# Optimization experiments

Hardware: AMD Instinct MI355X
Metric: run time of the kernel (lower is better)

Reference implementation:

```python
import jax, jax.numpy as jnp
import numpy as np

NUM_EMBEDDINGS = 1024
EMBEDDING_DIM = 64
COMMITMENT_COST = 0.25


def setup_inputs() -> dict:
    key = jax.random.key(0)
    k_x, k_cb = jax.random.split(key)
    x = jax.random.normal(k_x, (16, EMBEDDING_DIM, 64, 64), dtype=jnp.float32)
    # nn.Embedding weight init: uniform(-1/K, 1/K)
    codebook = jax.random.uniform(
        k_cb, (NUM_EMBEDDINGS, EMBEDDING_DIM), dtype=jnp.float32,
        minval=-1.0 / NUM_EMBEDDINGS, maxval=1.0 / NUM_EMBEDDINGS)
    return {"x": x, "codebook": codebook}


def reference(x, codebook):
    sg = jax.lax.stop_gradient
    # NCHW -> NHWC
    inputs = jnp.transpose(x, (0, 2, 3, 1))  # [B,H,W,D]
    in_shape = inputs.shape
    flat = inputs.reshape(-1, EMBEDDING_DIM)  # [N,D]
    # squared L2 distances to each codebook entry: [N,K]
    distances = (jnp.sum(flat ** 2, axis=1, keepdims=True)
                 + jnp.sum(codebook ** 2, axis=1)
                 - 2.0 * jnp.matmul(flat, codebook.T))
    encoding_indices = jnp.argmin(distances, axis=1)  # [N]
    # one-hot matmul in the original == plain gather
    quantized = codebook[encoding_indices].reshape(in_shape)  # [B,H,W,D]
    e_latent_loss = jnp.mean((sg(quantized) - inputs) ** 2)
    q_latent_loss = jnp.mean((quantized - sg(inputs)) ** 2)
    loss = q_latent_loss + COMMITMENT_COST * e_latent_loss
    # straight-through estimator
    quantized = inputs + sg(quantized - inputs)
    quantized = jnp.transpose(quantized, (0, 3, 1, 2))  # NHWC -> NCHW
    return quantized, loss
```

## Files before the change

### kernel.cpp

```cpp
#include <hip/hip_runtime.h>

#define NPTS   65536
#define DIM    64
#define KCODES 1024
#define HW     4096
#define ROWP   68

typedef __attribute__((ext_vector_type(8))) short  short8;
typedef __attribute__((ext_vector_type(4))) float  floatx4;
typedef __attribute__((ext_vector_type(2))) unsigned long long ull2;

__device__ __forceinline__ short f2bf(float f) {
    unsigned u = __builtin_bit_cast(unsigned, f);
    u = (u + 0x7FFFu + ((u >> 16) & 1u)) >> 16;
    return (short)u;
}
__device__ __forceinline__ float bf2f(short s) {
    unsigned u = ((unsigned)(unsigned short)s) << 16;
    return __builtin_bit_cast(float, u);
}

__global__ void vq_prep(const float* __restrict__ cb, float* __restrict__ cbn_nh,
                        float* __restrict__ loss_ptr) {
    int k = blockIdx.x * blockDim.x + threadIdx.x;
    if (k == 0) *loss_ptr = 0.0f;
    if (k < KCODES) {
        const float* row = cb + (size_t)k * DIM;
        float s = 0.0f;
        #pragma unroll
        for (int d = 0; d < DIM; ++d) s = fmaf(row[d], row[d], s);
        cbn_nh[k] = -0.5f * s;
    }
}

__global__ __launch_bounds__(256, 1) void vq_main(
    const float* __restrict__ x, const float* __restrict__ cb,
    const float* __restrict__ cbn_nh, float* __restrict__ out,
    float* __restrict__ loss_ptr)
{
    __shared__ __align__(16) short s_cb[KCODES * ROWP];
    __shared__ float s_cbn[KCODES];
    __shared__ int   s_idx[256];
    __shared__ float s_red[4];

    const int tid  = threadIdx.x;
    const int lane = tid & 63;
    const int wave = tid >> 6;
    const int col  = lane & 15;
    const int quad = lane >> 4;

    {
        const float4* src = (const float4*)cb;
        for (int i = 0; i < 64; ++i) {
            int f4 = tid + 256 * i;
            float4 v = src[f4];
            int e = f4 << 2;
            int code = e >> 6, within = e & 63;
            unsigned long long p =
                ((unsigned long long)(unsigned short)f2bf(v.x)) |
                ((unsigned long long)(unsigned short)f2bf(v.y) << 16) |
                ((unsigned long long)(unsigned short)f2bf(v.z) << 32) |
                ((unsigned long long)(unsigned short)f2bf(v.w) << 48);
            *(unsigned long long*)&s_cb[code * ROWP + within] = p;
        }
        #pragma unroll
        for (int i = 0; i < 4; ++i) s_cbn[tid + 256 * i] = cbn_nh[tid + 256 * i];
    }

    const int p0 = blockIdx.x * 256 + wave * 64;
    short8 afrag[4][2];
    #pragma unroll
    for (int blk = 0; blk < 4; ++blk) {
        int n = p0 + blk * 16 + col;
        const float* bp = x + ((size_t)(n >> 12) << 18) + (n & 4095);
        #pragma unroll
        for (int kh = 0; kh < 2; ++kh) {
            int dbase = kh * 32 + quad * 8;
            short8 f;
            #pragma unroll
            for (int j = 0; j < 8; ++j)
                f[j] = f2bf(bp[(size_t)(dbase + j) * HW]);
            afrag[blk][kh] = f;
        }
    }
    __syncthreads();

    float best[4][4];
    #pragma unroll
    for (int blk = 0; blk < 4; ++blk)
        #pragma unroll
        for (int r = 0; r < 4; ++r) best[blk][r] = -3.4e38f;

    for (int t = 0; t < 64; ++t) {
        const int cbase = t * 16;
        const int code  = cbase + col;
        const float initv = s_cbn[code];
        const unsigned idxv = (unsigned)code;
        const short* rp = &s_cb[code * ROWP + quad * 8];
        ull2 u0; u0.x = *(const unsigned long long*)rp;
        u0.y = *(const unsigned long long*)(rp + 4);
        ull2 u1; u1.x = *(const unsigned long long*)(rp + 32);
        u1.y = *(const unsigned long long*)(rp + 36);
        const short8 b0 = __builtin_bit_cast(short8, u0);
        const short8 b1 = __builtin_bit_cast(short8, u1);
        floatx4 cinit = {initv, initv, initv, initv};
        #pragma unroll
        for (int blk = 0; blk < 4; ++blk) {
            floatx4 acc = __builtin_amdgcn_mfma_f32_16x16x32_bf16(afrag[blk][0], b0, cinit, 0, 0, 0);
            acc = __builtin_amdgcn_mfma_f32_16x16x32_bf16(afrag[blk][1], b1, acc, 0, 0, 0);
            #pragma unroll
            for (int r = 0; r < 4; ++r) {
                unsigned pb = (__builtin_bit_cast(unsigned, acc[r]) & 0xFFFFFC00u) | idxv;
                best[blk][r] = fmaxf(best[blk][r], __builtin_bit_cast(float, pb));
            }
        }
    }

    #pragma unroll
    for (int blk = 0; blk < 4; ++blk)
        #pragma unroll
        for (int r = 0; r < 4; ++r) {
            float v = best[blk][r];
            v = fmaxf(v, __shfl_xor(v, 1, 64));
            v = fmaxf(v, __shfl_xor(v, 2, 64));
            v = fmaxf(v, __shfl_xor(v, 4, 64));
            v = fmaxf(v, __shfl_xor(v, 8, 64));
            best[blk][r] = v;
        }
    if (col == 0) {
        #pragma unroll
        for (int blk = 0; blk < 4; ++blk)
            #pragma unroll
            for (int r = 0; r < 4; ++r)
                s_idx[wave * 64 + blk * 16 + quad * 4 + r] =
                    (int)(__builtin_bit_cast(unsigned, best[blk][r]) & 1023u);
    }

    {
        int n = p0 + lane;
        int idx = s_idx[wave * 64 + lane];
        size_t base = ((size_t)(n >> 12) << 18) + (n & 4095);
        float* op = out + base;
        const float* xp = x + base;
        float lsum = 0.0f;
        #pragma unroll
        for (int j = 0; j < 16; ++j) {
            unsigned long long u = *(const unsigned long long*)&s_cb[idx * ROWP + j * 4];
            #pragma unroll
            for (int e = 0; e < 4; ++e) {
                float c = bf2f((short)(u >> (16 * e)));
                int d = j * 4 + e;
                float xv = xp[(size_t)d * HW];
                op[(size_t)d * HW] = c;
                float diff = xv - c;
                lsum = fmaf(diff, diff, lsum);
            }
        }
        #pragma unroll
        for (int off = 32; off > 0; off >>= 1)
            lsum += __shfl_down(lsum, off, 64);
        if (lane == 0) s_red[wave] = lsum;
    }
    __syncthreads();
    if (tid == 0) {
        float s = (s_red[0] + s_red[1]) + (s_red[2] + s_red[3]);
        atomicAdd(loss_ptr, s * (1.25f / (float)((size_t)NPTS * DIM)));
    }
}

extern "C" void kernel_launch(void* const* d_in, const int* in_sizes, int n_in,
                              void* d_out, int out_size, void* d_ws, size_t ws_size,
                              hipStream_t stream) {
    const float* x  = (const float*)d_in[0];
    const float* cb = (const float*)d_in[1];
    float* out      = (float*)d_out;
    float* cbn      = (float*)d_ws;
    float* loss_ptr = out + (size_t)NPTS * DIM;

    vq_prep<<<KCODES / 256, 256, 0, stream>>>(cb, cbn, loss_ptr);
    vq_main<<<NPTS / 256, 256, 0, stream>>>(x, cb, cbn, out, loss_ptr);
}
```

Measured before the change: 97.59 us.

## Use 1024-thread blocks with one 16-point tile per wave, fold norms in

Each block now runs 16 waves instead of 4. Every wave handles a single 16-point MFMA tile instead of four, which spreads the 256 points and the codebook staging over four times as many threads. The separate codebook-norm prep kernel is removed: the norms are computed from the bf16-rounded values during shared-memory staging using a shuffle reduction, and the prep kernel is replaced by a tiny loss-zeroing kernel. The epilogue splits the 64 dimensions across four thread groups. In exchange, each B-fragment loaded from LDS is now reused across only one tile instead of four, so LDS read traffic per MFMA roughly quadruples. The large block also needs an extra barrier and relies on occupancy that the ~140KB LDS footprint still limits to one block per CU.

```diff
diff --git a/kernel.cpp b/kernel.cpp
--- a/kernel.cpp
+++ b/kernel.cpp
@@ -20,28 +20,18 @@
     return __builtin_bit_cast(float, u);
 }
 
-__global__ void vq_prep(const float* __restrict__ cb, float* __restrict__ cbn_nh,
-                        float* __restrict__ loss_ptr) {
-    int k = blockIdx.x * blockDim.x + threadIdx.x;
-    if (k == 0) *loss_ptr = 0.0f;
-    if (k < KCODES) {
-        const float* row = cb + (size_t)k * DIM;
-        float s = 0.0f;
-        #pragma unroll
-        for (int d = 0; d < DIM; ++d) s = fmaf(row[d], row[d], s);
-        cbn_nh[k] = -0.5f * s;
-    }
+__global__ void vq_zero(float* __restrict__ loss_ptr) {
+    if (threadIdx.x == 0) *loss_ptr = 0.0f;
 }
 
-__global__ __launch_bounds__(256, 1) void vq_main(
+__global__ __launch_bounds__(1024, 4) void vq_main(
     const float* __restrict__ x, const float* __restrict__ cb,
-    const float* __restrict__ cbn_nh, float* __restrict__ out,
-    float* __restrict__ loss_ptr)
+    float* __restrict__ out, float* __restrict__ loss_ptr)
 {
     __shared__ __align__(16) short s_cb[KCODES * ROWP];
     __shared__ float s_cbn[KCODES];
     __shared__ int   s_idx[256];
-    __shared__ float s_red[4];
+    __shared__ float s_red[16];
 
     const int tid  = threadIdx.x;
     const int lane = tid & 63;
@@ -51,49 +41,46 @@
 
     {
         const float4* src = (const float4*)cb;
-        for (int i = 0; i < 64; ++i) {
-            int f4 = tid + 256 * i;
+        #pragma unroll
+        for (int i = 0; i < 16; ++i) {
+            int f4 = tid + 1024 * i;
             float4 v = src[f4];
-            int e = f4 << 2;
-            int code = e >> 6, within = e & 63;
+            short hx = f2bf(v.x), hy = f2bf(v.y), hz = f2bf(v.z), hw_ = f2bf(v.w);
             unsigned long long p =
-                ((unsigned long long)(unsigned short)f2bf(v.x)) |
-                ((unsigned long long)(unsigned short)f2bf(v.y) << 16) |
-                ((unsigned long long)(unsigned short)f2bf(v.z) << 32) |
-                ((unsigned long long)(unsigned short)f2bf(v.w) << 48);
-            *(unsigned long long*)&s_cb[code * ROWP + within] = p;
+                ((unsigned long long)(unsigned short)hx) |
+                ((unsigned long long)(unsigned short)hy << 16) |
+                ((unsigned long long)(unsigned short)hz << 32) |
+                ((unsigned long long)(unsigned short)hw_ << 48);
+            int code = f4 >> 4, w = f4 & 15;
+            *(unsigned long long*)&s_cb[code * ROWP + w * 4] = p;
+            float cx = bf2f(hx), cy = bf2f(hy), cz = bf2f(hz), cw = bf2f(hw_);
+            float ns = fmaf(cx, cx, fmaf(cy, cy, fmaf(cz, cz, cw * cw)));
+            ns += __shfl_xor(ns, 1, 64);
+            ns += __shfl_xor(ns, 2, 64);
+            ns += __shfl_xor(ns, 4, 64);
+            ns += __shfl_xor(ns, 8, 64);
+            if ((tid & 15) == 0) s_cbn[code] = -0.5f * ns;
         }
-        #pragma unroll
-        for (int i = 0; i < 4; ++i) s_cbn[tid + 256 * i] = cbn_nh[tid + 256 * i];
     }
 
-    const int p0 = blockIdx.x * 256 + wave * 64;
-    short8 afrag[4][2];
+    const int p0  = blockIdx.x * 256;
+    const int myn = p0 + wave * 16 + col;
+    const float* bp = x + ((size_t)(myn >> 12) << 18) + (myn & 4095);
+    short8 afrag[2];
     #pragma unroll
-    for (int blk = 0; blk < 4; ++blk) {
-        int n = p0 + blk * 16 + col;
-        const float* bp = x + ((size_t)(n >> 12) << 18) + (n & 4095);
+    for (int kh = 0; kh < 2; ++kh) {
+        int dbase = kh * 32 + quad * 8;
+        short8 f;
         #pragma unroll
-        for (int kh = 0; kh < 2; ++kh) {
-            int dbase = kh * 32 + quad * 8;
-            short8 f;
-            #pragma unroll
-            for (int j = 0; j < 8; ++j)
-                f[j] = f2bf(bp[(size_t)(dbase + j) * HW]);
-            afrag[blk][kh] = f;
-        }
+        for (int j = 0; j < 8; ++j)
+            f[j] = f2bf(bp[(size_t)(dbase + j) * HW]);
+        afrag[kh] = f;
     }
     __syncthreads();
 
-    float best[4][4];
-    #pragma unroll
-    for (int blk = 0; blk < 4; ++blk)
-        #pragma unroll
-        for (int r = 0; r < 4; ++r) best[blk][r] = -3.4e38f;
-
+    float best[4] = {-3.4e38f, -3.4e38f, -3.4e38f, -3.4e38f};
     for (int t = 0; t < 64; ++t) {
-        const int cbase = t * 16;
-        const int code  = cbase + col;
+        const int code = t * 16 + col;
         const float initv = s_cbn[code];
         const unsigned idxv = (unsigned)code;
         const short* rp = &s_cb[code * ROWP + quad * 8];
@@ -104,52 +91,47 @@
         const short8 b0 = __builtin_bit_cast(short8, u0);
         const short8 b1 = __builtin_bit_cast(short8, u1);
         floatx4 cinit = {initv, initv, initv, initv};
+        floatx4 acc = __builtin_amdgcn_mfma_f32_16x16x32_bf16(afrag[0], b0, cinit, 0, 0, 0);
+        acc = __builtin_amdgcn_mfma_f32_16x16x32_bf16(afrag[1], b1, acc, 0, 0, 0);
         #pragma unroll
-        for (int blk = 0; blk < 4; ++blk) {
-            floatx4 acc = __builtin_amdgcn_mfma_f32_16x16x32_bf16(afrag[blk][0], b0, cinit, 0, 0, 0);
-            acc = __builtin_amdgcn_mfma_f32_16x16x32_bf16(afrag[blk][1], b1, acc, 0, 0, 0);
-            #pragma unroll
-            for (int r = 0; r < 4; ++r) {
-                unsigned pb = (__builtin_bit_cast(unsigned, acc[r]) & 0xFFFFFC00u) | idxv;
-                best[blk][r] = fmaxf(best[blk][r], __builtin_bit_cast(float, pb));
-            }
+        for (int r = 0; r < 4; ++r) {
+            unsigned pb = (__builtin_bit_cast(unsigned, acc[r]) & 0xFFFFFC00u) | idxv;
+            best[r] = fmaxf(best[r], __builtin_bit_cast(float, pb));
         }
     }
 
     #pragma unroll
-    for (int blk = 0; blk < 4; ++blk)
-        #pragma unroll
-        for (int r = 0; r < 4; ++r) {
-            float v = best[blk][r];
-            v = fmaxf(v, __shfl_xor(v, 1, 64));
-            v = fmaxf(v, __shfl_xor(v, 2, 64));
-            v = fmaxf(v, __shfl_xor(v, 4, 64));
-            v = fmaxf(v, __shfl_xor(v, 8, 64));
-            best[blk][r] = v;
-        }
+    for (int r = 0; r < 4; ++r) {
+        float v = best[r];
+        v = fmaxf(v, __shfl_xor(v, 1, 64));
+        v = fmaxf(v, __shfl_xor(v, 2, 64));
+        v = fmaxf(v, __shfl_xor(v, 4, 64));
+        v = fmaxf(v, __shfl_xor(v, 8, 64));
+        best[r] = v;
+    }
     if (col == 0) {
         #pragma unroll
-        for (int blk = 0; blk < 4; ++blk)
-            #pragma unroll
-            for (int r = 0; r < 4; ++r)
-                s_idx[wave * 64 + blk * 16 + quad * 4 + r] =
-                    (int)(__builtin_bit_cast(unsigned, best[blk][r]) & 1023u);
+        for (int r = 0; r < 4; ++r)
+            s_idx[wave * 16 + quad * 4 + r] =
+                (int)(__builtin_bit_cast(unsigned, best[r]) & 1023u);
     }
+    __syncthreads();
 
     {
-        int n = p0 + lane;
-        int idx = s_idx[wave * 64 + lane];
+        int n   = p0 + (tid & 255);
+        int dq  = tid >> 8;
+        int idx = s_idx[tid & 255];
         size_t base = ((size_t)(n >> 12) << 18) + (n & 4095);
         float* op = out + base;
         const float* xp = x + base;
         float lsum = 0.0f;
         #pragma unroll
-        for (int j = 0; j < 16; ++j) {
-            unsigned long long u = *(const unsigned long long*)&s_cb[idx * ROWP + j * 4];
+        for (int j = 0; j < 4; ++j) {
+            unsigned long long u = *(const unsigned long long*)&s_cb[idx * ROWP + dq * 16 + j * 4];
             #pragma unroll
             for (int e = 0; e < 4; ++e) {
+                int d = dq * 16 + j * 4 + e;
                 float c = bf2f((short)(u >> (16 * e)));
-                int d = j * 4 + e;
                 float xv = xp[(size_t)d * HW];
                 op[(size_t)d * HW] = c;
                 float diff = xv - c;
@@ -163,7 +145,9 @@
     }
     __syncthreads();
     if (tid == 0) {
-        float s = (s_red[0] + s_red[1]) + (s_red[2] + s_red[3]);
+        float s = 0.0f;
+        #pragma unroll
+        for (int w = 0; w < 16; ++w) s += s_red[w];
         atomicAdd(loss_ptr, s * (1.25f / (float)((size_t)NPTS * DIM)));
     }
 }
@@ -174,9 +158,8 @@
     const float* x  = (const float*)d_in[0];
     const float* cb = (const float*)d_in[1];
     float* out      = (float*)d_out;
-    float* cbn      = (float*)d_ws;
     float* loss_ptr = out + (size_t)NPTS * DIM;
 
-    vq_prep<<<KCODES / 256, 256, 0, stream>>>(cb, cbn, loss_ptr);
-    vq_main<<<NPTS / 256, 256, 0, stream>>>(x, cb, cbn, out, loss_ptr);
+    vq_zero<<<1, 64, 0, stream>>>(loss_ptr);
+    vq_main<<<NPTS / 256, 1024, 0, stream>>>(x, cb, out, loss_ptr);
 }
```

Result: faster. 92.83 us (-4.9%).
